# Performance work log

Hardware: AMD Instinct MI355X
Metric: run time of the kernel (lower is better)

## Reference

```python
import jax, jax.numpy as jnp
import numpy as np

N, E, H, NH, RBF = 20000, 200000, 128, 8, 64
HD = H // NH
CUT_HI = 5.0


def _ln(t, s, b, eps=1e-6):
    mu = t.mean(-1, keepdims=True)
    var = ((t - mu) ** 2).mean(-1, keepdims=True)
    return (t - mu) * jax.lax.rsqrt(var + eps) * s + b


def _cutoff(w):
    # cosine cutoff, cutoff_lower = 0
    return 0.5 * (jnp.cos(w * (jnp.pi / CUT_HI)) + 1.0) * (w < CUT_HI)


def _xavier(k, fi, fo):
    lim = float(np.sqrt(6.0 / (fi + fo)))
    return jax.random.uniform(k, (fi, fo), minval=-lim, maxval=lim, dtype=jnp.float32)


def setup_inputs() -> dict:
    key = jax.random.key(0)
    ks = jax.random.split(key, 16)
    return {
        "x": jax.random.normal(ks[0], (N, H), jnp.float32),
        "vec": jax.random.normal(ks[1], (N, 3, H), jnp.float32),
        "edge_weight": jax.random.uniform(ks[2], (E, 1), jnp.float32) * 6.0,
        "edge_attr": jax.random.uniform(ks[3], (E, RBF), jnp.float32),
        "edge_vec": jax.random.normal(ks[4], (E, 3), jnp.float32),
        "senders": jax.random.randint(ks[5], (E,), 0, N, jnp.int32),
        "receivers": jax.random.randint(ks[6], (E,), 0, N, jnp.int32),
        "ln_s": jnp.ones((H,), jnp.float32), "ln_b": jnp.zeros((H,), jnp.float32),
        "Wq": _xavier(ks[7], H, H), "bq": jnp.zeros((H,), jnp.float32),
        "Wk": _xavier(ks[8], H, H), "bk": jnp.zeros((H,), jnp.float32),
        "Wv": _xavier(ks[9], H, 3 * H), "bv": jnp.zeros((3 * H,), jnp.float32),
        "Wvec": _xavier(ks[10], H, 3 * H),
        "Wdk": _xavier(ks[11], RBF, H), "bdk": jnp.zeros((H,), jnp.float32),
        "Wdv": _xavier(ks[12], RBF, 3 * H), "bdv": jnp.zeros((3 * H,), jnp.float32),
        "Wo": _xavier(ks[13], H, 3 * H), "bo": jnp.zeros((3 * H,), jnp.float32),
        "qln_s": jnp.ones((HD,), jnp.float32), "qln_b": jnp.zeros((HD,), jnp.float32),
        "kln_s": jnp.ones((HD,), jnp.float32), "kln_b": jnp.zeros((HD,), jnp.float32),
    }


def reference(x, vec, edge_weight, edge_attr, edge_vec, senders, receivers,
              ln_s, ln_b, Wq, bq, Wk, bk, Wv, bv, Wvec, Wdk, bdk, Wdv, bdv,
              Wo, bo, qln_s, qln_b, kln_s, kln_b):
    act = jax.nn.silu
    n = x.shape[0]
    xn = _ln(x, ln_s, ln_b)                                    # [N,H]
    q = _ln((xn @ Wq + bq).reshape(n, NH, HD), qln_s, qln_b)   # [N,h,d]
    k = _ln((xn @ Wk + bk).reshape(n, NH, HD), kln_s, kln_b)   # [N,h,d]
    v = (xn @ Wv + bv).reshape(n, NH, 3 * HD)                  # [N,h,3d]
    vp = vec @ Wvec                                            # [N,3,3H]
    vec1, vec2, vec3 = jnp.split(vp, 3, axis=-1)               # [N,3,H] each
    vec_dot = (vec1 * vec2).sum(axis=1)                        # [N,H]
    vec_h = vec.reshape(n, 3, NH, HD)                          # [N,3,h,d]
    dk = act(edge_attr @ Wdk + bdk).reshape(-1, NH, HD)        # [E,h,d]
    dv = act(edge_attr @ Wdv + bdv).reshape(-1, NH, 3 * HD)    # [E,h,3d]
    # message
    attn = (q[receivers] * k[senders] * dk).sum(axis=-1)       # [E,h]
    attn = act(attn) * _cutoff(edge_weight)                    # [E,h]
    v_j = v[senders] * dv                                      # [E,h,3d]
    xm, m1, m2 = jnp.split(v_j, 3, axis=2)                     # [E,h,d]
    xm = xm * attn[:, :, None]                                 # [E,h,d]
    vec_m = vec_h[senders] * m1[:, None] + m2[:, None] * edge_vec[:, :, None, None]  # [E,3,h,d]
    # aggregate
    x_agg = jax.ops.segment_sum(xm, receivers, num_segments=n).reshape(n, H)
    vec_agg = jax.ops.segment_sum(vec_m, receivers, num_segments=n).reshape(n, 3, H)
    o1, o2, o3 = jnp.split(x_agg @ Wo + bo, 3, axis=1)         # [N,H] each
    dvec = vec3 * o1[:, None] + vec_agg                        # [N,3,H]
    dx = vec_dot * o2 + o3                                     # [N,H]
    return (dx, dvec)
```

## Files before the change

### kernel.cpp

```cpp
#include <hip/hip_runtime.h>
#include <stdint.h>

#define NN 20000
#define NE 200000

typedef __attribute__((ext_vector_type(8))) short bf16x8;
typedef __attribute__((ext_vector_type(4))) float f32x4;

__device__ __forceinline__ float bf2f(uint32_t u) {
  union { uint32_t i; float f; } v; v.i = u << 16; return v.f;
}
__device__ __forceinline__ uint16_t f2bf(float f) {
  union { float f; uint32_t i; } v; v.f = f;
  return (uint16_t)((v.i + 0x7fffu + ((v.i >> 16) & 1u)) >> 16);
}
__device__ __forceinline__ uint32_t pk2(float lo, float hi) {
  return (uint32_t)f2bf(lo) | ((uint32_t)f2bf(hi) << 16);
}
__device__ __forceinline__ float siluf(float x) { return x / (1.f + __expf(-x)); }

__global__ void k_prep(const float* __restrict__ Wq, const float* __restrict__ Wk,
                       const float* __restrict__ Wv, const float* __restrict__ Wvec,
                       const float* __restrict__ Wdk, const float* __restrict__ Wdv,
                       const float* __restrict__ Wo, const float* __restrict__ bq,
                       const float* __restrict__ bk, const float* __restrict__ bv,
                       const float* __restrict__ bdk, const float* __restrict__ bdv,
                       uint16_t* __restrict__ WTqkv, uint16_t* __restrict__ WTvec,
                       uint16_t* __restrict__ WTdkv2, uint16_t* __restrict__ WTo,
                       float* __restrict__ Bqkv, float* __restrict__ Bdkv2) {
  int idx = blockIdx.x * 256 + threadIdx.x;
  if (idx < 98304) {
    int rr = idx >> 7, k = idx & 127;
    float v;
    if (rr < 128)      v = Wq[k * 128 + rr];
    else if (rr < 256) v = Wk[k * 128 + rr - 128];
    else {
      int j2 = rr - 256, j = j2 >> 2, c = j2 & 3;
      v = (c < 3) ? Wv[k * 384 + (j >> 4) * 48 + c * 16 + (j & 15)] : 0.f;
    }
    WTqkv[idx] = f2bf(v);
    return;
  }
  idx -= 98304;
  if (idx < 49152) {
    int c = idx >> 7, k = idx & 127;
    WTvec[idx] = f2bf(Wvec[k * 384 + c]);
    return;
  }
  idx -= 49152;
  if (idx < 32768) {
    int rr = idx >> 6, k = idx & 63;
    float v;
    if (rr < 128) v = Wdk[k * 128 + rr];
    else {
      int j = rr - 128, p = j >> 7, hd = j & 127;
      v = Wdv[k * 384 + (hd >> 4) * 48 + p * 16 + (hd & 15)];
    }
    WTdkv2[idx] = f2bf(v);
    return;
  }
  idx -= 32768;
  if (idx < 49152) {
    int c = idx >> 7, k = idx & 127;
    WTo[idx] = f2bf(Wo[k * 384 + c]);
    return;
  }
  idx -= 49152;
  if (idx < 768) {
    if (idx < 128)      Bqkv[idx] = bq[idx];
    else if (idx < 256) Bqkv[idx] = bk[idx - 128];
    else {
      int j2 = idx - 256, j = j2 >> 2, c = j2 & 3;
      Bqkv[idx] = (c < 3) ? bv[(j >> 4) * 48 + c * 16 + (j & 15)] : 0.f;
    }
  } else if (idx < 1280) {
    int t = idx - 768;
    if (t < 128) Bdkv2[t] = bdk[t];
    else {
      int j = t - 128, p = j >> 7, hd = j & 127;
      Bdkv2[t] = bdv[(hd >> 4) * 48 + p * 16 + (hd & 15)];
    }
  }
}

__global__ void k_node_pre(const float* __restrict__ x, const float* __restrict__ s,
                           const float* __restrict__ b, const float* __restrict__ vec,
                           uint16_t* __restrict__ xn_b, uint16_t* __restrict__ vec_b,
                           uint16_t* __restrict__ vec_w) {
  if (blockIdx.x < 5000) {
    int gt = blockIdx.x * 256 + threadIdx.x;
    int node = gt >> 6, lane = gt & 63;
    if (node >= NN) return;
    const float* row = x + (size_t)node * 128;
    float2 v = *(const float2*)&row[lane * 2];
    float sum = v.x + v.y, sq = v.x * v.x + v.y * v.y;
    #pragma unroll
    for (int off = 32; off; off >>= 1) { sum += __shfl_xor(sum, off); sq += __shfl_xor(sq, off); }
    float mu = sum * (1.f / 128.f);
    float var = sq * (1.f / 128.f) - mu * mu;
    float rs = rsqrtf(var + 1e-6f);
    float o0 = (v.x - mu) * rs * s[lane * 2] + b[lane * 2];
    float o1 = (v.y - mu) * rs * s[lane * 2 + 1] + b[lane * 2 + 1];
    ((uint32_t*)xn_b)[(size_t)node * 64 + lane] = pk2(o0, o1);
  } else if (blockIdx.x < 20000) {
    int i = (blockIdx.x - 5000) * 256 + threadIdx.x;
    float2 v = ((const float2*)vec)[i];
    ((uint32_t*)vec_b)[i] = pk2(v.x, v.y);
  } else {
    int i = (blockIdx.x - 20000) * 256 + threadIdx.x;
    int n = i >> 7, j = i & 127;
    const float* vr = vec + (size_t)n * 384 + j;
    uint2 o;
    o.x = pk2(vr[0], vr[128]);
    o.y = pk2(vr[256], 0.f);
    *(uint2*)&vec_w[(size_t)n * 512 + j * 4] = o;
  }
}

__global__ void k_cast_bf16(const float* __restrict__ src, uint16_t* __restrict__ dst, int npairs) {
  int i = blockIdx.x * 256 + threadIdx.x;
  if (i >= npairs) return;
  float2 v = ((const float2*)src)[i];
  ((uint32_t*)dst)[i] = pk2(v.x, v.y);
}

__global__ void k_hist(const int* __restrict__ rcv, int* __restrict__ deg) {
  int e = blockIdx.x * 256 + threadIdx.x;
  if (e < NE) atomicAdd(&deg[rcv[e]], 1);
}

__global__ void k_scan1(const int* __restrict__ deg, int* __restrict__ bsum) {
  __shared__ int ws[4];
  int i = blockIdx.x * 256 + threadIdx.x;
  int x = (i < NN) ? deg[i] : 0;
  #pragma unroll
  for (int d = 32; d; d >>= 1) x += __shfl_xor(x, d);
  if ((threadIdx.x & 63) == 0) ws[threadIdx.x >> 6] = x;
  __syncthreads();
  if (threadIdx.x == 0) bsum[blockIdx.x] = ws[0] + ws[1] + ws[2] + ws[3];
}

__global__ void k_scan2(int* __restrict__ bsum, int nb, int* __restrict__ off) {
  int lane = threadIdx.x;
  int carry = 0;
  for (int base = 0; base < nb; base += 64) {
    int i = base + lane;
    int x = (i < nb) ? bsum[i] : 0;
    int v = x;
    #pragma unroll
    for (int d = 1; d < 64; d <<= 1) { int y = __shfl_up(v, d); if (lane >= d) v += y; }
    if (i < nb) bsum[i] = carry + v - x;
    carry += __shfl(v, 63);
  }
  if (lane == 0) off[NN] = carry;
}

__global__ void k_scan3(const int* __restrict__ deg, const int* __restrict__ bsum,
                        int* __restrict__ off, int* __restrict__ cur) {
  __shared__ int ws[4];
  int t = threadIdx.x, lane = t & 63, w = t >> 6;
  int i = blockIdx.x * 256 + t;
  int x = (i < NN) ? deg[i] : 0;
  int v = x;
  #pragma unroll
  for (int d = 1; d < 64; d <<= 1) { int y = __shfl_up(v, d); if (lane >= d) v += y; }
  if (lane == 63) ws[w] = v;
  __syncthreads();
  int wadd = 0;
  for (int j = 0; j < w; j++) wadd += ws[j];
  int excl = bsum[blockIdx.x] + wadd + v - x;
  if (i < NN) { off[i] = excl; cur[i] = excl; }
}

__global__ void k_scatter(const int* __restrict__ rcv, int* __restrict__ cur,
                          int* __restrict__ perm) {
  int e = blockIdx.x * 256 + threadIdx.x;
  if (e >= NE) return;
  int pos = atomicAdd(&cur[rcv[e]], 1);
  perm[pos] = e;
}

__global__ void k_permute(const float* __restrict__ ea, const int* __restrict__ perm,
                          const int* __restrict__ snd, const int* __restrict__ rcv,
                          const float* __restrict__ ew, const float* __restrict__ evec,
                          uint16_t* __restrict__ ea_perm, int* __restrict__ sndp,
                          int* __restrict__ rcvp, float4* __restrict__ edata) {
  int idx = blockIdx.x * 256 + threadIdx.x;
  if (idx >= NE * 16) return;
  int i = idx >> 4, j = idx & 15;
  int e = perm[i];
  float4 v = *(const float4*)&ea[(size_t)e * 64 + j * 4];
  uint2 o;
  o.x = pk2(v.x, v.y);
  o.y = pk2(v.z, v.w);
  *(uint2*)&ea_perm[(size_t)i * 64 + j * 4] = o;
  if (j == 0) {
    sndp[i] = snd[e];
    rcvp[i] = rcv[e];
    float w = ew[e];
    float cut = (w < 5.f) ? 0.5f * (__cosf(w * 0.628318530717958648f) + 1.f) : 0.f;
    edata[i] = make_float4(evec[e * 3], evec[e * 3 + 1], evec[e * 3 + 2], cut);
  }
}

template <int KTOT, bool OUT_BF16, bool SILU>
__global__ __launch_bounds__(256) void k_gemm(const uint16_t* __restrict__ A,
                                              const uint16_t* __restrict__ BT,
                                              const float* __restrict__ bias,
                                              void* __restrict__ Cout, int M, int Fo) {
  __shared__ __align__(16) uint16_t As[128 * 72];
  __shared__ __align__(16) uint16_t Bs[128 * 72];
  int t = threadIdx.x;
  int l = t & 63;
  int row0 = blockIdx.y * 128, col0 = blockIdx.x * 128;
  int wm = ((t >> 6) >> 1) * 64, wn = ((t >> 6) & 1) * 64;
  f32x4 acc[4][4] = {};
  for (int kt = 0; kt < KTOT; kt += 64) {
    __syncthreads();
    #pragma unroll
    for (int i = 0; i < 4; i++) {
      int c = i * 256 + t;
      int row = c >> 3, ko = (c & 7) * 8;
      uint4 av = make_uint4(0u, 0u, 0u, 0u);
      int gr = row0 + row;
      if (gr < M) av = *(const uint4*)&A[(size_t)gr * KTOT + kt + ko];
      *(uint4*)&As[row * 72 + ko] = av;
      uint4 bw = *(const uint4*)&BT[(size_t)(col0 + row) * KTOT + kt + ko];
      *(uint4*)&Bs[row * 72 + ko] = bw;
    }
    __syncthreads();
    #pragma unroll
    for (int kk = 0; kk < 64; kk += 32) {
      bf16x8 af[4], bfr[4];
      #pragma unroll
      for (int mf = 0; mf < 4; mf++)
        af[mf] = *(const bf16x8*)&As[(wm + mf * 16 + (l & 15)) * 72 + (l >> 4) * 8 + kk];
      #pragma unroll
      for (int nf = 0; nf < 4; nf++)
        bfr[nf] = *(const bf16x8*)&Bs[(wn + nf * 16 + (l & 15)) * 72 + (l >> 4) * 8 + kk];
      #pragma unroll
      for (int mf = 0; mf < 4; mf++)
        #pragma unroll
        for (int nf = 0; nf < 4; nf++)
          acc[mf][nf] = __builtin_amdgcn_mfma_f32_16x16x32_bf16(af[mf], bfr[nf], acc[mf][nf], 0, 0, 0);
    }
  }
  float* Cf = (float*)Cout;
  uint16_t* Cb = (uint16_t*)Cout;
  #pragma unroll
  for (int mf = 0; mf < 4; mf++) {
    #pragma unroll
    for (int r = 0; r < 4; r++) {
      int grow = row0 + wm + mf * 16 + (l >> 4) * 4 + r;
      if (grow >= M) continue;
      #pragma unroll
      for (int nf = 0; nf < 4; nf++) {
        int gcol = col0 + wn + nf * 16 + (l & 15);
        float v = acc[mf][nf][r];
        if (bias) v += bias[gcol];
        if (SILU) v = siluf(v);
        if (OUT_BF16) Cb[(size_t)grow * Fo + gcol] = f2bf(v);
        else          Cf[(size_t)grow * Fo + gcol] = v;
      }
    }
  }
}

__global__ void k_headln(const uint16_t* __restrict__ qkv, const float* __restrict__ qs,
                         const float* __restrict__ qb, const float* __restrict__ ks,
                         const float* __restrict__ kb, uint16_t* __restrict__ out) {
  int idx = blockIdx.x * 256 + threadIdx.x;
  if (idx >= NN * 16) return;
  int n = idx >> 4, ph = idx & 15, part = ph >> 3, h = ph & 7;
  const uint16_t* src = qkv + (size_t)n * 768 + part * 128 + h * 16;
  float v[16], sum = 0.f;
  #pragma unroll
  for (int i = 0; i < 16; i++) { v[i] = bf2f(src[i]); sum += v[i]; }
  float mu = sum * (1.f / 16.f), var = 0.f;
  #pragma unroll
  for (int i = 0; i < 16; i++) { float dd = v[i] - mu; var += dd * dd; }
  float rs = rsqrtf(var * (1.f / 16.f) + 1e-6f);
  const float* sc = part ? ks : qs;
  const float* bb = part ? kb : qb;
  uint16_t* dst = out + (size_t)n * 256 + part * 128 + h * 16;
  #pragma unroll
  for (int i = 0; i < 16; i++) dst[i] = f2bf((v[i] - mu) * rs * sc[i] + bb[i]);
}

#define MTS 516

__device__ __forceinline__ void mfma32(const uint16_t* As, int r0,
                                       const uint16_t* __restrict__ BT2, int cb,
                                       int wn, int l, f32x4 acc[2][2]) {
  #pragma unroll
  for (int kk = 0; kk < 2; kk++) {
    bf16x8 af[2];
    #pragma unroll
    for (int mf = 0; mf < 2; mf++)
      af[mf] = *(const bf16x8*)&As[(r0 + mf * 16 + (l & 15)) * 68 + (l >> 4) * 8 + kk * 32];
    #pragma unroll
    for (int nf = 0; nf < 2; nf++) {
      bf16x8 bv = *(const bf16x8*)&BT2[(size_t)(cb * 128 + wn + nf * 16 + (l & 15)) * 64 +
                                       (l >> 4) * 8 + kk * 32];
      #pragma unroll
      for (int mf = 0; mf < 2; mf++)
        acc[mf][nf] = __builtin_amdgcn_mfma_f32_16x16x32_bf16(af[mf], bv, acc[mf][nf], 0, 0, 0);
    }
  }
}

__device__ __forceinline__ void silu_slot(uint16_t* mt, const float bsv[2], int slot,
                                          int wn, int l, f32x4 acc[2][2]) {
  #pragma unroll
  for (int mf = 0; mf < 2; mf++)
    #pragma unroll
    for (int r = 0; r < 4; r++) {
      int row = mf * 16 + (l >> 4) * 4 + r;
      #pragma unroll
      for (int nf = 0; nf < 2; nf++) {
        int c = wn + nf * 16 + (l & 15);
        mt[row * MTS + c * 4 + slot] = f2bf(siluf(acc[mf][nf][r] + bsv[nf]));
      }
    }
}

__global__ __launch_bounds__(256) void k_edge_all(
    const uint16_t* __restrict__ eap, const int* __restrict__ sndp,
    const int* __restrict__ rcvp, const int* __restrict__ off,
    const float4* __restrict__ edata, const uint16_t* __restrict__ WT2,
    const float* __restrict__ Bd2, const uint16_t* __restrict__ qk_b,
    const uint16_t* __restrict__ qkv_b, const uint16_t* __restrict__ vec_w,
    float* __restrict__ xagg, float* __restrict__ vecagg) {
  __shared__ __align__(16) uint16_t As[64 * 68];
  __shared__ __align__(16) uint16_t mt[32 * MTS];
  __shared__ float attn_l[32 * 8];
  __shared__ int sndl[64], rcvl[64], lo_g[64], hi_g[64];
  __shared__ float4 ed4[64];

  int e0 = blockIdx.x * 64;
  int t = threadIdx.x, l = t & 63, wn = (t >> 6) * 32;

  if (t < 64) {
    int e = e0 + t;
    int r = rcvp[e];
    sndl[t] = sndp[e]; rcvl[t] = r;
    lo_g[t] = off[r]; hi_g[t] = off[r + 1];
    ed4[t] = edata[e];
  }
  #pragma unroll
  for (int i = 0; i < 2; i++) {
    int c = i * 256 + t;
    int row = c >> 3, ko = (c & 7) * 8;
    *(uint4*)&As[row * 68 + ko] = *(const uint4*)&eap[(size_t)(e0 + row) * 64 + ko];
  }
  float bs[4][2];
  #pragma unroll
  for (int cb = 0; cb < 4; cb++) {
    bs[cb][0] = Bd2[cb * 128 + wn + (l & 15)];
    bs[cb][1] = Bd2[cb * 128 + wn + 16 + (l & 15)];
  }
  __syncthreads();

  #pragma unroll
  for (int half = 0; half < 2; half++) {
    int r0 = half * 32;
    { f32x4 acc[2][2] = {}; mfma32(As, r0, WT2, 0, wn, l, acc); silu_slot(mt, bs[0], 3, wn, l, acc); }
    __syncthreads();
    {
      int el = t >> 3, h = t & 7;
      int ge = r0 + el;
      int rn = rcvl[ge], sn = sndl[ge];
      const uint16_t* qb_ = qk_b + (size_t)rn * 256 + h * 16;
      const uint16_t* kb_ = qk_b + (size_t)sn * 256 + 128 + h * 16;
      uint4 q0 = *(const uint4*)qb_;
      uint4 q1 = *(const uint4*)(qb_ + 8);
      uint4 k0 = *(const uint4*)kb_;
      uint4 k1 = *(const uint4*)(kb_ + 8);
      { f32x4 acc[2][2] = {}; mfma32(As, r0, WT2, 1, wn, l, acc); silu_slot(mt, bs[1], 0, wn, l, acc); }
      { f32x4 acc[2][2] = {}; mfma32(As, r0, WT2, 2, wn, l, acc); silu_slot(mt, bs[2], 1, wn, l, acc); }
      { f32x4 acc[2][2] = {}; mfma32(As, r0, WT2, 3, wn, l, acc); silu_slot(mt, bs[3], 2, wn, l, acc); }
      const uint16_t* dkr = &mt[el * MTS + h * 64 + 3];
      uint32_t qa[8] = {q0.x, q0.y, q0.z, q0.w, q1.x, q1.y, q1.z, q1.w};
      uint32_t ka[8] = {k0.x, k0.y, k0.z, k0.w, k1.x, k1.y, k1.z, k1.w};
      float dot = 0.f;
      #pragma unroll
      for (int j = 0; j < 8; j++) {
        dot += bf2f(qa[j] & 0xffffu) * bf2f(ka[j] & 0xffffu) * bf2f(dkr[j * 8]);
        dot += bf2f(qa[j] >> 16)     * bf2f(ka[j] >> 16)     * bf2f(dkr[j * 8 + 4]);
      }
      attn_l[el * 8 + h] = siluf(dot) * ed4[ge].w;
    }
    __syncthreads();
    {
      int col = t & 127, sub = t >> 7;
      int i0 = r0 + sub * 16, i1 = i0 + 16;
      int ha = col >> 4;
      float accx = 0.f, a0 = 0.f, a1 = 0.f, a2 = 0.f;
      #pragma unroll 8
      for (int i = i0; i < i1; i++) {
        int li = i - r0;
        int n = rcvl[i], s = sndl[i];
        uint2 vt = *(const uint2*)&qkv_b[(size_t)s * 768 + 256 + col * 4];
        uint2 wt = *(const uint2*)&vec_w[(size_t)s * 512 + col * 4];
        uint2 mr = *(const uint2*)&mt[li * MTS + col * 4];
        float a = attn_l[li * 8 + ha];
        float xmv = bf2f(mr.x & 0xffffu), m1v = bf2f(mr.x >> 16), m2v = bf2f(mr.y & 0xffffu);
        accx += bf2f(vt.x & 0xffffu) * xmv * a;
        float mm1 = bf2f(vt.x >> 16) * m1v;
        float mm2 = bf2f(vt.y & 0xffffu) * m2v;
        float4 ev = ed4[i];
        a0 += bf2f(wt.x & 0xffffu) * mm1 + ev.x * mm2;
        a1 += bf2f(wt.x >> 16)     * mm1 + ev.y * mm2;
        a2 += bf2f(wt.y & 0xffffu) * mm1 + ev.z * mm2;
        if (i == i1 - 1 || rcvl[i + 1] != n) {
          bool cont = (lo_g[i] >= e0 + i0) && (hi_g[i] <= e0 + i1);
          float* dx_ = &xagg[(size_t)n * 128 + col];
          float* d0 = &vecagg[((size_t)n * 3 + 0) * 128 + col];
          float* d1 = &vecagg[((size_t)n * 3 + 1) * 128 + col];
          float* d2 = &vecagg[((size_t)n * 3 + 2) * 128 + col];
          if (cont) { *dx_ = accx; *d0 = a0; *d1 = a1; *d2 = a2; }
          else { atomicAdd(dx_, accx); atomicAdd(d0, a0); atomicAdd(d1, a1); atomicAdd(d2, a2); }
          accx = a0 = a1 = a2 = 0.f;
        }
      }
    }
    __syncthreads();
  }
}

__global__ void k_final(const float* __restrict__ o, const uint16_t* __restrict__ vp,
                        float* __restrict__ dx, float* __restrict__ dvec) {
  int idx = blockIdx.x * 256 + threadIdx.x;
  if (idx >= NN * 128) return;
  int n = idx >> 7, j = idx & 127;
  const float* op = o + (size_t)n * 384;
  float o1 = op[j], o2 = op[128 + j], o3 = op[256 + j];
  const uint16_t* vpn = vp + (size_t)n * 3 * 384;
  float vd = 0.f;
  #pragma unroll
  for (int c = 0; c < 3; c++)
    vd += bf2f(vpn[c * 384 + j]) * bf2f(vpn[c * 384 + 128 + j]);
  dx[idx] = vd * o2 + o3;
  #pragma unroll
  for (int c = 0; c < 3; c++) {
    size_t vi = ((size_t)n * 3 + c) * 128 + j;
    dvec[vi] = bf2f(vpn[c * 384 + 256 + j]) * o1 + dvec[vi];
  }
}

static inline int cdiv_i(long long a, long long b) { return (int)((a + b - 1) / b); }

extern "C" void kernel_launch(void* const* d_in, const int* in_sizes, int n_in,
                              void* d_out, int out_size, void* d_ws, size_t ws_size,
                              hipStream_t stream) {
  const float* x    = (const float*)d_in[0];
  const float* vec  = (const float*)d_in[1];
  const float* ew   = (const float*)d_in[2];
  const float* ea   = (const float*)d_in[3];
  const float* evec = (const float*)d_in[4];
  const int*   snd  = (const int*)d_in[5];
  const int*   rcv  = (const int*)d_in[6];
  const float* ln_s = (const float*)d_in[7];
  const float* ln_b = (const float*)d_in[8];
  const float* Wq = (const float*)d_in[9];   const float* bq = (const float*)d_in[10];
  const float* Wk = (const float*)d_in[11];  const float* bk = (const float*)d_in[12];
  const float* Wv = (const float*)d_in[13];  const float* bv = (const float*)d_in[14];
  const float* Wvec = (const float*)d_in[15];
  const float* Wdk = (const float*)d_in[16]; const float* bdk = (const float*)d_in[17];
  const float* Wdv = (const float*)d_in[18]; const float* bdv = (const float*)d_in[19];
  const float* Wo = (const float*)d_in[20];  const float* bo = (const float*)d_in[21];
  const float* qln_s = (const float*)d_in[22]; const float* qln_b = (const float*)d_in[23];
  const float* kln_s = (const float*)d_in[24]; const float* kln_b = (const float*)d_in[25];
  (void)in_sizes; (void)n_in; (void)ws_size;

  uint8_t* p = (uint8_t*)d_ws;
  auto alloc = [&](size_t bytes) -> uint8_t* {
    uint8_t* r = p; p += (bytes + 255) & ~(size_t)255; return r;
  };
  uint16_t* WTqkv = (uint16_t*)alloc(768 * 128 * 2);
  float*    Bqkv  = (float*)alloc(768 * 4);
  uint16_t* WTvec = (uint16_t*)alloc(384 * 128 * 2);
  uint16_t* WTdkv = (uint16_t*)alloc(512 * 64 * 2);
  float*    Bdkv  = (float*)alloc(512 * 4);
  uint16_t* WTo   = (uint16_t*)alloc(384 * 128 * 2);
  int*      deg   = (int*)alloc(NN * 4);
  int*      off   = (int*)alloc((NN + 1) * 4);
  int*      cur   = (int*)alloc(NN * 4);
  int*      bsum  = (int*)alloc(256 * 4);
  int*      perm  = (int*)alloc((size_t)NE * 4);
  int*      sndp  = (int*)alloc((size_t)NE * 4);
  int*      rcvp  = (int*)alloc((size_t)NE * 4);
  float4*   edata = (float4*)alloc((size_t)NE * 16);
  uint16_t* ea_perm = (uint16_t*)alloc((size_t)NE * 64 * 2);
  uint16_t* xn_b  = (uint16_t*)alloc((size_t)NN * 128 * 2);
  uint16_t* qkv_b = (uint16_t*)alloc((size_t)NN * 768 * 2);
  uint16_t* qk_b  = (uint16_t*)alloc((size_t)NN * 256 * 2);
  uint16_t* vec_b = (uint16_t*)alloc((size_t)NN * 3 * 128 * 2);
  uint16_t* vec_w = (uint16_t*)alloc((size_t)NN * 512 * 2);
  uint16_t* vp    = (uint16_t*)alloc((size_t)NN * 3 * 384 * 2);
  float*    o      = (float*)alloc((size_t)NN * 384 * 4);
  uint16_t* xagg_b = (uint16_t*)alloc((size_t)NN * 128 * 2);

  float* xagg   = (float*)d_out;
  float* vecagg = (float*)d_out + (size_t)NN * 128;

  hipMemsetAsync(d_out, 0, (size_t)out_size * 4, stream);

  k_prep<<<cdiv_i(98304 + 49152 + 32768 + 49152 + 1280, 256), 256, 0, stream>>>(
      Wq, Wk, Wv, Wvec, Wdk, Wdv, Wo, bq, bk, bv, bdk, bdv,
      WTqkv, WTvec, WTdkv, WTo, Bqkv, Bdkv);

  int NSB = cdiv_i(NN, 256);
  hipMemsetAsync(deg, 0, NN * 4, stream);
  k_hist<<<cdiv_i(NE, 256), 256, 0, stream>>>(rcv, deg);
  k_scan1<<<NSB, 256, 0, stream>>>(deg, bsum);
  k_scan2<<<1, 64, 0, stream>>>(bsum, NSB, off);
  k_scan3<<<NSB, 256, 0, stream>>>(deg, bsum, off, cur);
  k_scatter<<<cdiv_i(NE, 256), 256, 0, stream>>>(rcv, cur, perm);
  k_permute<<<cdiv_i((long long)NE * 16, 256), 256, 0, stream>>>(ea, perm, snd, rcv, ew, evec,
                                                                 ea_perm, sndp, rcvp, edata);

  k_node_pre<<<30000, 256, 0, stream>>>(x, ln_s, ln_b, vec, xn_b, vec_b, vec_w);

  { dim3 g(768 / 128, cdiv_i(NN, 128));
    k_gemm<128, true, false><<<g, 256, 0, stream>>>(xn_b, WTqkv, Bqkv, qkv_b, NN, 768); }
  k_headln<<<cdiv_i((long long)NN * 16, 256), 256, 0, stream>>>(qkv_b, qln_s, qln_b, kln_s, kln_b, qk_b);

  { dim3 g(384 / 128, cdiv_i((long long)NN * 3, 128));
    k_gemm<128, true, false><<<g, 256, 0, stream>>>(vec_b, WTvec, nullptr, vp, NN * 3, 384); }

  k_edge_all<<<NE / 64, 256, 0, stream>>>(ea_perm, sndp, rcvp, off, edata, WTdkv, Bdkv,
                                          qk_b, qkv_b, vec_w, xagg, vecagg);

  k_cast_bf16<<<cdiv_i((long long)NN * 64, 256), 256, 0, stream>>>(xagg, xagg_b, NN * 64);
  { dim3 g(384 / 128, cdiv_i(NN, 128));
    k_gemm<128, false, false><<<g, 256, 0, stream>>>(xagg_b, WTo, bo, o, NN, 384); }

  k_final<<<cdiv_i((long long)NN * 128, 256), 256, 0, stream>>>(o, vp, xagg, vecagg);
}
```

Measured before the change: 347.9 us.

## Fuse head layernorm into QKV GEMM, interleave v and vec gather, drop cast kernels

Result: no change. 354.4 us (+1.8%).

```diff
diff --git a/kernel.cpp b/kernel.cpp
--- a/kernel.cpp
+++ b/kernel.cpp
@@ -18,6 +18,10 @@
   return (uint32_t)f2bf(lo) | ((uint32_t)f2bf(hi) << 16);
 }
 __device__ __forceinline__ float siluf(float x) { return x / (1.f + __expf(-x)); }
+__device__ __forceinline__ float prod2(uint32_t q2, uint32_t k2, uint32_t d2) {
+  return bf2f(q2 & 0xffffu) * bf2f(k2 & 0xffffu) * bf2f(d2 & 0xffffu)
+       + bf2f(q2 >> 16) * bf2f(k2 >> 16) * bf2f(d2 >> 16);
+}
 
 __global__ void k_prep(const float* __restrict__ Wq, const float* __restrict__ Wk,
                        const float* __restrict__ Wv, const float* __restrict__ Wvec,
@@ -85,8 +89,7 @@
 
 __global__ void k_node_pre(const float* __restrict__ x, const float* __restrict__ s,
                            const float* __restrict__ b, const float* __restrict__ vec,
-                           uint16_t* __restrict__ xn_b, uint16_t* __restrict__ vec_b,
-                           uint16_t* __restrict__ vec_w) {
+                           uint16_t* __restrict__ xn_b, uint16_t* __restrict__ combo) {
   if (blockIdx.x < 5000) {
     int gt = blockIdx.x * 256 + threadIdx.x;
     int node = gt >> 6, lane = gt & 63;
@@ -102,26 +105,16 @@
     float o0 = (v.x - mu) * rs * s[lane * 2] + b[lane * 2];
     float o1 = (v.y - mu) * rs * s[lane * 2 + 1] + b[lane * 2 + 1];
     ((uint32_t*)xn_b)[(size_t)node * 64 + lane] = pk2(o0, o1);
-  } else if (blockIdx.x < 20000) {
+  } else {
     int i = (blockIdx.x - 5000) * 256 + threadIdx.x;
-    float2 v = ((const float2*)vec)[i];
-    ((uint32_t*)vec_b)[i] = pk2(v.x, v.y);
-  } else {
-    int i = (blockIdx.x - 20000) * 256 + threadIdx.x;
+    if (i >= NN * 128) return;
     int n = i >> 7, j = i & 127;
     const float* vr = vec + (size_t)n * 384 + j;
     uint2 o;
     o.x = pk2(vr[0], vr[128]);
     o.y = pk2(vr[256], 0.f);
-    *(uint2*)&vec_w[(size_t)n * 512 + j * 4] = o;
-  }
-}
-
-__global__ void k_cast_bf16(const float* __restrict__ src, uint16_t* __restrict__ dst, int npairs) {
-  int i = blockIdx.x * 256 + threadIdx.x;
-  if (i >= npairs) return;
-  float2 v = ((const float2*)src)[i];
-  ((uint32_t*)dst)[i] = pk2(v.x, v.y);
+    *(uint2*)&combo[(size_t)n * 1024 + j * 8 + 4] = o;
+  }
 }
 
 __global__ void k_hist(const int* __restrict__ rcv, int* __restrict__ deg) {
@@ -203,13 +196,15 @@
   }
 }
 
-template <int KTOT, bool OUT_BF16, bool SILU>
-__global__ __launch_bounds__(256) void k_gemm(const uint16_t* __restrict__ A,
+template <int KTOT, bool OUT_BF16, bool SILU, bool AF32>
+__global__ __launch_bounds__(256) void k_gemm(const void* __restrict__ A,
                                               const uint16_t* __restrict__ BT,
                                               const float* __restrict__ bias,
                                               void* __restrict__ Cout, int M, int Fo) {
   __shared__ __align__(16) uint16_t As[128 * 72];
   __shared__ __align__(16) uint16_t Bs[128 * 72];
+  const uint16_t* A16 = (const uint16_t*)A;
+  const float* A32 = (const float*)A;
   int t = threadIdx.x;
   int l = t & 63;
   int row0 = blockIdx.y * 128, col0 = blockIdx.x * 128;
@@ -223,7 +218,15 @@
       int row = c >> 3, ko = (c & 7) * 8;
       uint4 av = make_uint4(0u, 0u, 0u, 0u);
       int gr = row0 + row;
-      if (gr < M) av = *(const uint4*)&A[(size_t)gr * KTOT + kt + ko];
+      if (gr < M) {
+        if (AF32) {
+          float4 f0 = *(const float4*)&A32[(size_t)gr * KTOT + kt + ko];
+          float4 f1 = *(const float4*)&A32[(size_t)gr * KTOT + kt + ko + 4];
+          av = make_uint4(pk2(f0.x, f0.y), pk2(f0.z, f0.w), pk2(f1.x, f1.y), pk2(f1.z, f1.w));
+        } else {
+          av = *(const uint4*)&A16[(size_t)gr * KTOT + kt + ko];
+        }
+      }
       *(uint4*)&As[row * 72 + ko] = av;
       uint4 bw = *(const uint4*)&BT[(size_t)(col0 + row) * KTOT + kt + ko];
       *(uint4*)&Bs[row * 72 + ko] = bw;
@@ -266,25 +269,94 @@
   }
 }
 
-__global__ void k_headln(const uint16_t* __restrict__ qkv, const float* __restrict__ qs,
-                         const float* __restrict__ qb, const float* __restrict__ ks,
-                         const float* __restrict__ kb, uint16_t* __restrict__ out) {
-  int idx = blockIdx.x * 256 + threadIdx.x;
-  if (idx >= NN * 16) return;
-  int n = idx >> 4, ph = idx & 15, part = ph >> 3, h = ph & 7;
-  const uint16_t* src = qkv + (size_t)n * 768 + part * 128 + h * 16;
-  float v[16], sum = 0.f;
-  #pragma unroll
-  for (int i = 0; i < 16; i++) { v[i] = bf2f(src[i]); sum += v[i]; }
-  float mu = sum * (1.f / 16.f), var = 0.f;
-  #pragma unroll
-  for (int i = 0; i < 16; i++) { float dd = v[i] - mu; var += dd * dd; }
-  float rs = rsqrtf(var * (1.f / 16.f) + 1e-6f);
-  const float* sc = part ? ks : qs;
-  const float* bb = part ? kb : qb;
-  uint16_t* dst = out + (size_t)n * 256 + part * 128 + h * 16;
-  #pragma unroll
-  for (int i = 0; i < 16; i++) dst[i] = f2bf((v[i] - mu) * rs * sc[i] + bb[i]);
+__global__ __launch_bounds__(256) void k_gemm_qkv(
+    const uint16_t* __restrict__ A, const uint16_t* __restrict__ BT,
+    const float* __restrict__ bias, const float* __restrict__ qs,
+    const float* __restrict__ qb, const float* __restrict__ ks,
+    const float* __restrict__ kb, uint16_t* __restrict__ qk_b,
+    uint16_t* __restrict__ combo) {
+  __shared__ __align__(16) uint16_t As[128 * 72];
+  __shared__ __align__(16) uint16_t Bs[128 * 72];
+  int t = threadIdx.x;
+  int l = t & 63;
+  int row0 = blockIdx.y * 128, col0 = blockIdx.x * 128;
+  int wm = ((t >> 6) >> 1) * 64, wn = ((t >> 6) & 1) * 64;
+  f32x4 acc[4][4] = {};
+  for (int kt = 0; kt < 128; kt += 64) {
+    __syncthreads();
+    #pragma unroll
+    for (int i = 0; i < 4; i++) {
+      int c = i * 256 + t;
+      int row = c >> 3, ko = (c & 7) * 8;
+      uint4 av = make_uint4(0u, 0u, 0u, 0u);
+      int gr = row0 + row;
+      if (gr < NN) av = *(const uint4*)&A[(size_t)gr * 128 + kt + ko];
+      *(uint4*)&As[row * 72 + ko] = av;
+      uint4 bw = *(const uint4*)&BT[(size_t)(col0 + row) * 128 + kt + ko];
+      *(uint4*)&Bs[row * 72 + ko] = bw;
+    }
+    __syncthreads();
+    #pragma unroll
+    for (int kk = 0; kk < 64; kk += 32) {
+      bf16x8 af[4], bfr[4];
+      #pragma unroll
+      for (int mf = 0; mf < 4; mf++)
+        af[mf] = *(const bf16x8*)&As[(wm + mf * 16 + (l & 15)) * 72 + (l >> 4) * 8 + kk];
+      #pragma unroll
+      for (int nf = 0; nf < 4; nf++)
+        bfr[nf] = *(const bf16x8*)&Bs[(wn + nf * 16 + (l & 15)) * 72 + (l >> 4) * 8 + kk];
+      #pragma unroll
+      for (int mf = 0; mf < 4; mf++)
+        #pragma unroll
+        for (int nf = 0; nf < 4; nf++)
+          acc[mf][nf] = __builtin_amdgcn_mfma_f32_16x16x32_bf16(af[mf], bfr[nf], acc[mf][nf], 0, 0, 0);
+    }
+  }
+  int d = l & 15;
+  if (col0 < 256) {
+    float sc_q = qs[d], bb_q = qb[d], sc_k = ks[d], bb_k = kb[d];
+    #pragma unroll
+    for (int mf = 0; mf < 4; mf++) {
+      #pragma unroll
+      for (int r = 0; r < 4; r++) {
+        int grow = row0 + wm + mf * 16 + (l >> 4) * 4 + r;
+        bool ok = grow < NN;
+        #pragma unroll
+        for (int nf = 0; nf < 4; nf++) {
+          int gcol = col0 + wn + nf * 16 + d;
+          float v = acc[mf][nf][r] + bias[gcol];
+          float s1 = v;
+          s1 += __shfl_xor(s1, 1); s1 += __shfl_xor(s1, 2);
+          s1 += __shfl_xor(s1, 4); s1 += __shfl_xor(s1, 8);
+          float mu = s1 * (1.f / 16.f);
+          float dd = v - mu;
+          float s2 = dd * dd;
+          s2 += __shfl_xor(s2, 1); s2 += __shfl_xor(s2, 2);
+          s2 += __shfl_xor(s2, 4); s2 += __shfl_xor(s2, 8);
+          float rs = rsqrtf(s2 * (1.f / 16.f) + 1e-6f);
+          bool isq = gcol < 128;
+          float ov = dd * rs * (isq ? sc_q : sc_k) + (isq ? bb_q : bb_k);
+          if (ok) qk_b[(size_t)grow * 256 + gcol] = f2bf(ov);
+        }
+      }
+    }
+  } else {
+    #pragma unroll
+    for (int mf = 0; mf < 4; mf++) {
+      #pragma unroll
+      for (int r = 0; r < 4; r++) {
+        int grow = row0 + wm + mf * 16 + (l >> 4) * 4 + r;
+        if (grow >= NN) continue;
+        #pragma unroll
+        for (int nf = 0; nf < 4; nf++) {
+          int gcol = col0 + wn + nf * 16 + d;
+          int j2 = gcol - 256, j = j2 >> 2, c = j2 & 3;
+          if (c < 3)
+            combo[(size_t)grow * 1024 + j * 8 + c] = f2bf(acc[mf][nf][r] + bias[gcol]);
+        }
+      }
+    }
+  }
 }
 
 #define MTS 516
@@ -320,6 +392,21 @@
       for (int nf = 0; nf < 2; nf++) {
         int c = wn + nf * 16 + (l & 15);
         mt[row * MTS + c * 4 + slot] = f2bf(siluf(acc[mf][nf][r] + bsv[nf]));
+      }
+    }
+}
+
+__device__ __forceinline__ void silu_dk(uint16_t* mtd, const float bsv[2],
+                                        int wn, int l, f32x4 acc[2][2]) {
+  #pragma unroll
+  for (int mf = 0; mf < 2; mf++)
+    #pragma unroll
+    for (int r = 0; r < 4; r++) {
+      int row = mf * 16 + (l >> 4) * 4 + r;
+      #pragma unroll
+      for (int nf = 0; nf < 2; nf++) {
+        int c = wn + nf * 16 + (l & 15);
+        mtd[row * 140 + c] = f2bf(siluf(acc[mf][nf][r] + bsv[nf]));
       }
     }
 }
@@ -329,10 +416,11 @@
     const int* __restrict__ rcvp, const int* __restrict__ off,
     const float4* __restrict__ edata, const uint16_t* __restrict__ WT2,
     const float* __restrict__ Bd2, const uint16_t* __restrict__ qk_b,
-    const uint16_t* __restrict__ qkv_b, const uint16_t* __restrict__ vec_w,
-    float* __restrict__ xagg, float* __restrict__ vecagg) {
+    const uint16_t* __restrict__ combo, float* __restrict__ xagg,
+    float* __restrict__ vecagg) {
   __shared__ __align__(16) uint16_t As[64 * 68];
   __shared__ __align__(16) uint16_t mt[32 * MTS];
+  __shared__ __align__(16) uint16_t mtd[32 * 140];
   __shared__ float attn_l[32 * 8];
   __shared__ int sndl[64], rcvl[64], lo_g[64], hi_g[64];
   __shared__ float4 ed4[64];
@@ -364,7 +452,7 @@
   #pragma unroll
   for (int half = 0; half < 2; half++) {
     int r0 = half * 32;
-    { f32x4 acc[2][2] = {}; mfma32(As, r0, WT2, 0, wn, l, acc); silu_slot(mt, bs[0], 3, wn, l, acc); }
+    { f32x4 acc[2][2] = {}; mfma32(As, r0, WT2, 0, wn, l, acc); silu_dk(mtd, bs[0], wn, l, acc); }
     __syncthreads();
     {
       int el = t >> 3, h = t & 7;
@@ -379,15 +467,12 @@
       { f32x4 acc[2][2] = {}; mfma32(As, r0, WT2, 1, wn, l, acc); silu_slot(mt, bs[1], 0, wn, l, acc); }
       { f32x4 acc[2][2] = {}; mfma32(As, r0, WT2, 2, wn, l, acc); silu_slot(mt, bs[2], 1, wn, l, acc); }
       { f32x4 acc[2][2] = {}; mfma32(As, r0, WT2, 3, wn, l, acc); silu_slot(mt, bs[3], 2, wn, l, acc); }
-      const uint16_t* dkr = &mt[el * MTS + h * 64 + 3];
+      const uint32_t* dp = (const uint32_t*)&mtd[el * 140 + h * 16];
       uint32_t qa[8] = {q0.x, q0.y, q0.z, q0.w, q1.x, q1.y, q1.z, q1.w};
       uint32_t ka[8] = {k0.x, k0.y, k0.z, k0.w, k1.x, k1.y, k1.z, k1.w};
       float dot = 0.f;
       #pragma unroll
-      for (int j = 0; j < 8; j++) {
-        dot += bf2f(qa[j] & 0xffffu) * bf2f(ka[j] & 0xffffu) * bf2f(dkr[j * 8]);
-        dot += bf2f(qa[j] >> 16)     * bf2f(ka[j] >> 16)     * bf2f(dkr[j * 8 + 4]);
-      }
+      for (int j = 0; j < 8; j++) dot += prod2(qa[j], ka[j], dp[j]);
       attn_l[el * 8 + h] = siluf(dot) * ed4[ge].w;
     }
     __syncthreads();
@@ -400,18 +485,17 @@
       for (int i = i0; i < i1; i++) {
         int li = i - r0;
         int n = rcvl[i], s = sndl[i];
-        uint2 vt = *(const uint2*)&qkv_b[(size_t)s * 768 + 256 + col * 4];
-        uint2 wt = *(const uint2*)&vec_w[(size_t)s * 512 + col * 4];
+        uint4 cv = *(const uint4*)&combo[(size_t)s * 1024 + col * 8];
         uint2 mr = *(const uint2*)&mt[li * MTS + col * 4];
         float a = attn_l[li * 8 + ha];
         float xmv = bf2f(mr.x & 0xffffu), m1v = bf2f(mr.x >> 16), m2v = bf2f(mr.y & 0xffffu);
-        accx += bf2f(vt.x & 0xffffu) * xmv * a;
-        float mm1 = bf2f(vt.x >> 16) * m1v;
-        float mm2 = bf2f(vt.y & 0xffffu) * m2v;
+        accx += bf2f(cv.x & 0xffffu) * xmv * a;
+        float mm1 = bf2f(cv.x >> 16) * m1v;
+        float mm2 = bf2f(cv.y & 0xffffu) * m2v;
         float4 ev = ed4[i];
-        a0 += bf2f(wt.x & 0xffffu) * mm1 + ev.x * mm2;
-        a1 += bf2f(wt.x >> 16)     * mm1 + ev.y * mm2;
-        a2 += bf2f(wt.y & 0xffffu) * mm1 + ev.z * mm2;
+        a0 += bf2f(cv.z & 0xffffu) * mm1 + ev.x * mm2;
+        a1 += bf2f(cv.z >> 16)     * mm1 + ev.y * mm2;
+        a2 += bf2f(cv.w & 0xffffu) * mm1 + ev.z * mm2;
         if (i == i1 - 1 || rcvl[i + 1] != n) {
           bool cont = (lo_g[i] >= e0 + i0) && (hi_g[i] <= e0 + i1);
           float* dx_ = &xagg[(size_t)n * 128 + col];
@@ -493,13 +577,10 @@
   float4*   edata = (float4*)alloc((size_t)NE * 16);
   uint16_t* ea_perm = (uint16_t*)alloc((size_t)NE * 64 * 2);
   uint16_t* xn_b  = (uint16_t*)alloc((size_t)NN * 128 * 2);
-  uint16_t* qkv_b = (uint16_t*)alloc((size_t)NN * 768 * 2);
+  uint16_t* combo = (uint16_t*)alloc((size_t)NN * 1024 * 2);
   uint16_t* qk_b  = (uint16_t*)alloc((size_t)NN * 256 * 2);
-  uint16_t* vec_b = (uint16_t*)alloc((size_t)NN * 3 * 128 * 2);
-  uint16_t* vec_w = (uint16_t*)alloc((size_t)NN * 512 * 2);
   uint16_t* vp    = (uint16_t*)alloc((size_t)NN * 3 * 384 * 2);
-  float*    o      = (float*)alloc((size_t)NN * 384 * 4);
-  uint16_t* xagg_b = (uint16_t*)alloc((size_t)NN * 128 * 2);
+  float*    o     = (float*)alloc((size_t)NN * 384 * 4);
 
   float* xagg   = (float*)d_out;
   float* vecagg = (float*)d_out + (size_t)NN * 128;
@@ -520,21 +601,21 @@
   k_permute<<<cdiv_i((long long)NE * 16, 256), 256, 0, stream>>>(ea, perm, snd, rcv, ew, evec,
                                                                  ea_perm, sndp, rcvp, edata);
 
-  k_node_pre<<<30000, 256, 0, stream>>>(x, ln_s, ln_b, vec, xn_b, vec_b, vec_w);
-
-  { dim3 g(768 / 128, cdiv_i(NN, 128));
-    k_gemm<128, true, false><<<g, 256, 0, stream>>>(xn_b, WTqkv, Bqkv, qkv_b, NN, 768); }
-  k_headln<<<cdiv_i((long long)NN * 16, 256), 256, 0, stream>>>(qkv_b, qln_s, qln_b, kln_s, kln_b, qk_b);
+  k_node_pre<<<5000 + cdiv_i((long long)NN * 128, 256), 256, 0, stream>>>(
+      x, ln_s, ln_b, vec, xn_b, combo);
+
+  { dim3 g(6, cdiv_i(NN, 128));
+    k_gemm_qkv<<<g, 256, 0, stream>>>(xn_b, WTqkv, Bqkv, qln_s, qln_b, kln_s, kln_b,
+                                      qk_b, combo); }
 
   { dim3 g(384 / 128, cdiv_i((long long)NN * 3, 128));
-    k_gemm<128, true, false><<<g, 256, 0, stream>>>(vec_b, WTvec, nullptr, vp, NN * 3, 384); }
+    k_gemm<128, true, false, true><<<g, 256, 0, stream>>>(vec, WTvec, nullptr, vp, NN * 3, 384); }
 
   k_edge_all<<<NE / 64, 256, 0, stream>>>(ea_perm, sndp, rcvp, off, edata, WTdkv, Bdkv,
-                                          qk_b, qkv_b, vec_w, xagg, vecagg);
-
-  k_cast_bf16<<<cdiv_i((long long)NN * 64, 256), 256, 0, stream>>>(xagg, xagg_b, NN * 64);
+                                          qk_b, combo, xagg, vecagg);
+
   { dim3 g(384 / 128, cdiv_i(NN, 128));
-    k_gemm<128, false, false><<<g, 256, 0, stream>>>(xagg_b, WTo, bo, o, NN, 384); }
+    k_gemm<128, false, false, true><<<g, 256, 0, stream>>>(xagg, WTo, bo, o, NN, 384); }
 
   k_final<<<cdiv_i((long long)NN * 128, 256), 256, 0, stream>>>(o, vp, xagg, vecagg);
 }
```
